# Performance work log

Measured on AMD Instinct MI355X. Metric: run time of the kernel, lower is better.

Reference implementation:

```python
import jax, jax.numpy as jnp
import numpy as np

H = 8  # n_heads (init_kwarg, closed over)


def setup_inputs() -> dict:
    key = jax.random.key(0)
    ks = jax.random.split(key, 5)
    B, T, D, L = 8, 4096, 512, 128
    # lecun_normal: std = 1/sqrt(fan_in), fan_in = first dim here
    X = jax.random.normal(ks[0], (B, T, D), dtype=jnp.float32)
    Wk = jax.random.normal(ks[1], (D, L), dtype=jnp.float32) / np.sqrt(D)
    Wq = jax.random.normal(ks[2], (D, L), dtype=jnp.float32) / np.sqrt(D)
    Wv = jax.random.normal(ks[3], (D, D), dtype=jnp.float32) / np.sqrt(D)
    o_proj = jax.random.normal(ks[4], (D, D), dtype=jnp.float32) / np.sqrt(D)
    return {"X": X, "Wk": Wk, "Wq": Wq, "Wv": Wv, "o_proj": o_proj}


def reference(X, Wk, Wq, Wv, o_proj):
    B, T, D = X.shape
    L = Wk.shape[1]
    Dh, Lh = D // H, L // H
    # time-major projections: (T, B, H, *)
    V = jnp.einsum('DM,BTD->TBM', Wv, X).reshape(T, B, H, Dh)
    Q = jnp.einsum('DL,BTD->TBL', Wq, X).reshape(T, B, H, Lh)
    K = jnp.einsum('DL,BTD->TBL', Wk, X).reshape(T, B, H, Lh)
    scale = jax.lax.rsqrt(jnp.array(Dh, dtype=jnp.float32))
    K_exp = jnp.exp(K * scale)                      # (T,B,H,Lh)
    alpha = jnp.cumsum(K_exp, axis=0)               # causal normalizer
    Qs = jax.nn.softmax(Q * scale, axis=-1) / alpha # (T,B,H,Lh)

    def step(carry, args):
        qs_t, ke_t, v_t = args
        carry = carry + jnp.einsum('bhl,bhd->bhld', ke_t, v_t)
        y_t = jnp.einsum('bhl,bhld->bhd', qs_t, carry)
        return carry, y_t

    init = jnp.zeros((B, H, Lh, Dh), dtype=X.dtype)
    _, y = jax.lax.scan(step, init, (Qs, K_exp, V), unroll=16)  # y: (T,B,H,Dh)
    # faithful to source: transpose(3,0,1,2) then reshape(B,T,D)
    y = y.transpose(3, 0, 1, 2).reshape(B, T, D)
    return y @ o_proj
```

## Files before the change

### kernel.cpp

```cpp
#include <hip/hip_runtime.h>
#include <hip/hip_bf16.h>

#define B_ 8
#define T_ 4096
#define D_ 512
#define L_ 128
#define H_ 8
#define Dh_ 64
#define Lh_ 16
#define M_ (B_*T_)
#define SCALE 0.125f

typedef __bf16 v8bf __attribute__((ext_vector_type(8)));
typedef float  v4f  __attribute__((ext_vector_type(4)));
typedef unsigned short u16;
typedef u16 v8u __attribute__((ext_vector_type(8)));

__device__ __forceinline__ float b2f(u16 h){
    unsigned int u = ((unsigned int)h) << 16;
    return __builtin_bit_cast(float, u);
}
__device__ __forceinline__ u16 f2bf(float f){
    unsigned int u = __builtin_bit_cast(unsigned int, f);
    u += 0x7FFFu + ((u >> 16) & 1u);
    return (u16)(u >> 16);
}

__global__ __launch_bounds__(256) void f32_to_bf16(
        const float* __restrict__ src, u16* __restrict__ dst)
{
    const size_t i = (size_t)blockIdx.x * 256 + threadIdx.x;
    const float4* s = (const float4*)src + i * 2;
    float4 a = s[0], b = s[1];
    v8u o;
    o[0] = f2bf(a.x); o[1] = f2bf(a.y); o[2] = f2bf(a.z); o[3] = f2bf(a.w);
    o[4] = f2bf(b.x); o[5] = f2bf(b.y); o[6] = f2bf(b.z); o[7] = f2bf(b.w);
    *((v8u*)dst + i) = o;
}

__global__ __launch_bounds__(256) void transpose_w(
        const float* __restrict__ src, u16* __restrict__ dst, int rows, int cols)
{
    __shared__ u16 tile[32][33];
    int tx = threadIdx.x, ty = threadIdx.y;
    int c0 = blockIdx.x * 32, r0 = blockIdx.y * 32;
    #pragma unroll
    for (int i = 0; i < 32; i += 8)
        tile[ty + i][tx] = f2bf(src[(size_t)(r0 + ty + i) * cols + c0 + tx]);
    __syncthreads();
    #pragma unroll
    for (int i = 0; i < 32; i += 8)
        dst[(size_t)(c0 + ty + i) * rows + r0 + tx] = tile[tx][ty + i];
}

template<int MODE>
__global__ __launch_bounds__(256) void gemm_mfma(
        const u16* __restrict__ A, const u16* __restrict__ Bt,
        float* __restrict__ Qo, u16* __restrict__ KEo,
        u16* __restrict__ Vo, float* __restrict__ OutF)
{
    __shared__ __align__(16) u16 As[128][48];
    __shared__ __align__(16) u16 Bs[128][48];
    const int tid  = threadIdx.x;
    const int wave = tid >> 6, lane = tid & 63;
    const int wm = wave >> 1, wn = wave & 1;
    const int lm = lane & 15, quad = lane >> 4;
    const int gm0 = blockIdx.x * 128, gn0 = blockIdx.y * 128;

    v4f acc[4][4];
    #pragma unroll
    for (int i = 0; i < 4; i++)
        #pragma unroll
        for (int j = 0; j < 4; j++)
            acc[i][j] = (v4f){0.f, 0.f, 0.f, 0.f};

    for (int kt = 0; kt < 16; ++kt) {
        const int k0 = kt * 32;
        #pragma unroll
        for (int rep = 0; rep < 2; ++rep) {
            int lin = tid + rep * 256;
            int r = lin >> 2, c8 = (lin & 3) * 8;
            *(v8u*)&As[r][c8] = *(const v8u*)&A [(size_t)(gm0 + r) * 512 + k0 + c8];
            *(v8u*)&Bs[r][c8] = *(const v8u*)&Bt[(size_t)(gn0 + r) * 512 + k0 + c8];
        }
        __syncthreads();
        v8bf af[4], bfr[4];
        #pragma unroll
        for (int mi = 0; mi < 4; mi++)
            af[mi] = *(const v8bf*)&As[wm * 64 + mi * 16 + lm][quad * 8];
        #pragma unroll
        for (int ni = 0; ni < 4; ni++)
            bfr[ni] = *(const v8bf*)&Bs[wn * 64 + ni * 16 + lm][quad * 8];
        #pragma unroll
        for (int mi = 0; mi < 4; mi++)
            #pragma unroll
            for (int ni = 0; ni < 4; ni++)
                acc[mi][ni] = __builtin_amdgcn_mfma_f32_16x16x32_bf16(
                                  af[mi], bfr[ni], acc[mi][ni], 0, 0, 0);
        __syncthreads();
    }

    #pragma unroll
    for (int mi = 0; mi < 4; mi++)
      #pragma unroll
      for (int ni = 0; ni < 4; ni++)
        #pragma unroll
        for (int i = 0; i < 4; i++) {
            int row = gm0 + wm * 64 + mi * 16 + quad * 4 + i;
            int col = gn0 + wn * 64 + ni * 16 + lm;
            float v = acc[mi][ni][i];
            if (MODE == 0) {
                if (col < 128)        Qo [(size_t)row * 128 + col]       = v;
                else if (col < 256)   KEo[(size_t)row * 128 + col - 128] = f2bf(__expf(v * SCALE));
                else                  Vo [(size_t)row * 512 + col - 256] = f2bf(v);
            } else {
                OutF[(size_t)row * 512 + col] = v;
            }
        }
}

__global__ __launch_bounds__(256, 2) void chunk_sums_mfma(
        const u16* __restrict__ KE, const u16* __restrict__ V,
        float* __restrict__ Mc, float* __restrict__ AB)
{
    struct CLDS { u16 KA[16][72]; u16 VT[64][72]; };
    __shared__ __align__(16) CLDS lds[4];
    const int tid = threadIdx.x, wave = tid >> 6, lane = tid & 63;
    const int lm = lane & 15, quad = lane >> 4;
    const int ch = blockIdx.x * 4 + wave;
    const int bh = ch >> 6, c = ch & 63, b = bh >> 3, h = bh & 7;
    const int t0 = b * T_ + c * 64;
    CLDS& L = lds[wave];

    {
        const u16* kp = KE + (size_t)(t0 + lane) * L_ + h * Lh_;
        v8u k0 = *(const v8u*)kp, k1 = *(const v8u*)(kp + 8);
        #pragma unroll
        for (int l = 0; l < 8; l++) L.KA[l][lane]     = k0[l];
        #pragma unroll
        for (int l = 0; l < 8; l++) L.KA[l + 8][lane] = k1[l];
        const u16* vp = V + (size_t)(t0 + lane) * D_ + h * Dh_;
        #pragma unroll
        for (int seg = 0; seg < 8; ++seg) {
            v8u pv = *(const v8u*)(vp + seg * 8);
            #pragma unroll
            for (int j = 0; j < 8; j++) L.VT[seg * 8 + j][lane] = pv[j];
        }
    }
    __syncthreads();

    v8bf ka[2];
    #pragma unroll
    for (int ki = 0; ki < 2; ki++)
        ka[ki] = *(const v8bf*)&L.KA[lm][ki * 32 + quad * 8];

    v8u onesu;
    #pragma unroll
    for (int j = 0; j < 8; j++) onesu[j] = 0x3F80;
    v8bf ones = __builtin_bit_cast(v8bf, onesu);

    v4f accL = (v4f){0.f, 0.f, 0.f, 0.f};
    accL = __builtin_amdgcn_mfma_f32_16x16x32_bf16(ka[0], ones, accL, 0, 0, 0);
    accL = __builtin_amdgcn_mfma_f32_16x16x32_bf16(ka[1], ones, accL, 0, 0, 0);

    v4f accM[4];
    #pragma unroll
    for (int nd = 0; nd < 4; nd++) accM[nd] = (v4f){0.f, 0.f, 0.f, 0.f};
    #pragma unroll
    for (int nd = 0; nd < 4; nd++)
        #pragma unroll
        for (int ki = 0; ki < 2; ki++) {
            v8bf vb = *(const v8bf*)&L.VT[nd * 16 + lm][ki * 32 + quad * 8];
            accM[nd] = __builtin_amdgcn_mfma_f32_16x16x32_bf16(ka[ki], vb, accM[nd], 0, 0, 0);
        }

    float* mcb = Mc + (size_t)ch * 1024;
    #pragma unroll
    for (int nd = 0; nd < 4; nd++)
        #pragma unroll
        for (int i = 0; i < 4; i++)
            mcb[(quad * 4 + i) * 64 + nd * 16 + lm] = accM[nd][i];
    if (lm == 0) {
        #pragma unroll
        for (int i = 0; i < 4; i++) AB[ch * 16 + quad * 4 + i] = accL[i];
    }
}

__global__ __launch_bounds__(256) void chunk_prefix(
        float* __restrict__ Mc, float* __restrict__ AB)
{
    const int bh = blockIdx.x >> 2, qq = blockIdx.x & 3;
    const int i = qq * 256 + threadIdx.x;
    float run = 0.f;
    for (int c = 0; c < 64; ++c) {
        size_t off = ((size_t)(bh * 64 + c)) * 1024 + i;
        float m = Mc[off]; Mc[off] = run; run += m;
    }
    if (qq == 0 && threadIdx.x < 16) {
        float r2 = 0.f; const int l = threadIdx.x;
        for (int c = 0; c < 64; ++c) {
            int off = (bh * 64 + c) * 16 + l;
            float a = AB[off]; AB[off] = r2; r2 += a;
        }
    }
}

__global__ __launch_bounds__(256, 2) void intra_mfma(
        const float* __restrict__ Q, const u16* __restrict__ KE,
        const u16* __restrict__ V, const float* __restrict__ Mc,
        const float* __restrict__ AB, u16* __restrict__ Y)
{
    struct ILDS {
        union {
            struct { u16 KA[16][72]; u16 Sc[16][72]; u16 qs[64][40]; } s;
            u16 p[64][72];
        } r;
        u16 VT[64][72];
    };
    __shared__ __align__(16) ILDS lds[4];
    const int tid = threadIdx.x, wave = tid >> 6, lane = tid & 63;
    const int lm = lane & 15, quad = lane >> 4;
    const int ch = blockIdx.x * 4 + wave;
    const int bh = ch >> 6, c = ch & 63, b = bh >> 3, h = bh & 7;
    const int t0 = b * T_ + c * 64;
    ILDS& L = lds[wave];

    {
        const u16* kp = KE + (size_t)(t0 + lane) * L_ + h * Lh_;
        v8u k0 = *(const v8u*)kp, k1 = *(const v8u*)(kp + 8);
        #pragma unroll
        for (int l = 0; l < 8; l++) L.r.s.KA[l][lane]     = k0[l];
        #pragma unroll
        for (int l = 0; l < 8; l++) L.r.s.KA[l + 8][lane] = k1[l];
        const u16* vp = V + (size_t)(t0 + lane) * D_ + h * Dh_;
        #pragma unroll
        for (int seg = 0; seg < 8; ++seg) {
            v8u pv = *(const v8u*)(vp + seg * 8);
            #pragma unroll
            for (int j = 0; j < 8; j++) L.VT[seg * 8 + j][lane] = pv[j];
        }
        const float* mcb = Mc + (size_t)ch * 1024;
        #pragma unroll
        for (int l = 0; l < 16; l++)
            L.r.s.Sc[l][lane] = f2bf(mcb[l * 64 + lane]);
        v8u z8;
        #pragma unroll
        for (int j = 0; j < 8; j++) z8[j] = 0;
        *(v8u*)&L.r.s.qs[lane][16] = z8;
        *(v8u*)&L.r.s.qs[lane][24] = z8;
    }
    const float ab = AB[ch * 16 + lm];
    __syncthreads();

    v4f acc_a[4];
    #pragma unroll
    for (int mi = 0; mi < 4; mi++) acc_a[mi] = (v4f){ab, ab, ab, ab};
    #pragma unroll
    for (int mi = 0; mi < 4; mi++)
        #pragma unroll
        for (int ki = 0; ki < 2; ki++) {
            if (ki == 1 && mi < 2) continue;
            v8u ta;
            #pragma unroll
            for (int j = 0; j < 8; j++)
                ta[j] = (ki * 32 + quad * 8 + j <= mi * 16 + lm) ? (u16)0x3F80 : (u16)0;
            v8bf kb = *(const v8bf*)&L.r.s.KA[lm][ki * 32 + quad * 8];
            acc_a[mi] = __builtin_amdgcn_mfma_f32_16x16x32_bf16(
                            __builtin_bit_cast(v8bf, ta), kb, acc_a[mi], 0, 0, 0);
        }

    #pragma unroll
    for (int mi = 0; mi < 4; mi++)
        #pragma unroll
        for (int i = 0; i < 4; i++) {
            int t = mi * 16 + quad * 4 + i;
            float qv = Q[(size_t)(t0 + t) * L_ + h * Lh_ + lm] * SCALE;
            float m = qv;
            #pragma unroll
            for (int off = 1; off < 16; off <<= 1) m = fmaxf(m, __shfl_xor(m, off));
            float e = __expf(qv - m);
            float s = e;
            #pragma unroll
            for (int off = 1; off < 16; off <<= 1) s += __shfl_xor(s, off);
            L.r.s.qs[t][lm] = f2bf(e / (s * acc_a[mi][i]));
        }
    __syncthreads();

    v8bf aq[4];
    #pragma unroll
    for (int mi = 0; mi < 4; mi++)
        aq[mi] = *(const v8bf*)&L.r.s.qs[mi * 16 + lm][quad * 8];

    v4f accP[4][4], accY[4][4];
    #pragma unroll
    for (int mi = 0; mi < 4; mi++)
        #pragma unroll
        for (int ni = 0; ni < 4; ni++) {
            accP[mi][ni] = (v4f){0.f, 0.f, 0.f, 0.f};
            accY[mi][ni] = (v4f){0.f, 0.f, 0.f, 0.f};
        }

    #pragma unroll
    for (int ni = 0; ni < 4; ni++) {
        v8u kbu;
        #pragma unroll
        for (int j = 0; j < 8; j++) kbu[j] = 0;
        if (quad < 2) {
            #pragma unroll
            for (int j = 0; j < 8; j++)
                kbu[j] = L.r.s.KA[quad * 8 + j][ni * 16 + lm];
        }
        v8bf kbf = __builtin_bit_cast(v8bf, kbu);
        #pragma unroll
        for (int mi = ni; mi < 4; mi++)
            accP[mi][ni] = __builtin_amdgcn_mfma_f32_16x16x32_bf16(
                               aq[mi], kbf, accP[mi][ni], 0, 0, 0);
    }
    #pragma unroll
    for (int nd = 0; nd < 4; nd++) {
        v8u scu;
        #pragma unroll
        for (int j = 0; j < 8; j++) scu[j] = 0;
        if (quad < 2) {
            #pragma unroll
            for (int j = 0; j < 8; j++)
                scu[j] = L.r.s.Sc[quad * 8 + j][nd * 16 + lm];
        }
        v8bf scf = __builtin_bit_cast(v8bf, scu);
        #pragma unroll
        for (int mi = 0; mi < 4; mi++)
            accY[mi][nd] = __builtin_amdgcn_mfma_f32_16x16x32_bf16(
                               aq[mi], scf, accY[mi][nd], 0, 0, 0);
    }
    __syncthreads();

    #pragma unroll
    for (int mi = 0; mi < 4; mi++)
        #pragma unroll
        for (int ni = 0; ni < 4; ni++)
            #pragma unroll
            for (int i = 0; i < 4; i++) {
                int t = mi * 16 + quad * 4 + i, tp = ni * 16 + lm;
                float pv = (ni < mi) ? accP[mi][ni][i]
                          : (ni == mi ? ((tp <= t) ? accP[mi][ni][i] : 0.f) : 0.f);
                L.r.p[t][tp] = f2bf(pv);
            }
    __syncthreads();

    v8bf vb[4][2];
    #pragma unroll
    for (int nd = 0; nd < 4; nd++)
        #pragma unroll
        for (int ki = 0; ki < 2; ki++)
            vb[nd][ki] = *(const v8bf*)&L.VT[nd * 16 + lm][ki * 32 + quad * 8];
    #pragma unroll
    for (int mi = 0; mi < 4; mi++)
        #pragma unroll
        for (int ki = 0; ki < 2; ki++) {
            if (ki == 1 && mi < 2) continue;
            v8bf pa = *(const v8bf*)&L.r.p[mi * 16 + lm][ki * 32 + quad * 8];
            #pragma unroll
            for (int nd = 0; nd < 4; nd++)
                accY[mi][nd] = __builtin_amdgcn_mfma_f32_16x16x32_bf16(
                                   pa, vb[nd][ki], accY[mi][nd], 0, 0, 0);
        }

    #pragma unroll
    for (int mi = 0; mi < 4; mi++)
        #pragma unroll
        for (int nd = 0; nd < 4; nd++)
            #pragma unroll
            for (int i = 0; i < 4; i++) {
                int t = mi * 16 + quad * 4 + i;
                Y[(((size_t)(c * 64 + t)) * 64 + bh) * 64 + nd * 16 + lm] =
                    f2bf(accY[mi][nd][i]);
            }
}

__global__ __launch_bounds__(64) void transpose_Y(
        const u16* __restrict__ Y, u16* __restrict__ Z)
{
    __shared__ __align__(16) u16 tile[64][72];
    const int g = blockIdx.x;
    const int t = threadIdx.x;
    const u16* yp = Y + ((size_t)(g * 64 + t)) * 64;
    #pragma unroll
    for (int seg = 0; seg < 8; ++seg)
        *(v8u*)&tile[t][seg * 8] = *(const v8u*)(yp + seg * 8);
    __syncthreads();
    const int d = t;
    u16* zp = Z + (size_t)d * 262144 + (size_t)g * 64;
    #pragma unroll
    for (int seg = 0; seg < 8; ++seg) {
        v8u pk;
        #pragma unroll
        for (int j = 0; j < 8; j++) pk[j] = tile[seg * 8 + j][d];
        *(v8u*)(zp + seg * 8) = pk;
    }
}

extern "C" void kernel_launch(void* const* d_in, const int* in_sizes, int n_in,
                              void* d_out, int out_size, void* d_ws, size_t ws_size,
                              hipStream_t stream)
{
    (void)in_sizes; (void)n_in; (void)out_size; (void)ws_size;
    const float* X  = (const float*)d_in[0];
    const float* Wk = (const float*)d_in[1];
    const float* Wq = (const float*)d_in[2];
    const float* Wv = (const float*)d_in[3];
    const float* Wo = (const float*)d_in[4];
    float* Out = (float*)d_out;

    char* p = (char*)d_ws;
    auto alloc = [&](size_t bytes) { char* r = p; p += (bytes + 255) & ~(size_t)255; return r; };
    u16*   Xb = (u16*)  alloc((size_t)M_ * 512 * 2);
    u16*   WT = (u16*)  alloc((size_t)768 * 512 * 2);
    u16*   OT = (u16*)  alloc((size_t)512 * 512 * 2);
    u16*   V  = (u16*)  alloc((size_t)M_ * 512 * 2);
    float* Mc = (float*)alloc((size_t)4096 * 1024 * 4);
    float* AB = (float*)alloc((size_t)4096 * 16 * 4);
    float* Q  = (float*)alloc((size_t)M_ * 128 * 4);
    u16*   KE = (u16*)  alloc((size_t)M_ * 128 * 2);
    u16*   Y  = (u16*)  alloc((size_t)M_ * 512 * 2);
    u16*   Z  = (u16*)Mc;

    f32_to_bf16<<<8192, 256, 0, stream>>>(X, Xb);

    dim3 tb(32, 8);
    transpose_w<<<dim3(4, 16),  tb, 0, stream>>>(Wq, WT + 0   * 512, 512, 128);
    transpose_w<<<dim3(4, 16),  tb, 0, stream>>>(Wk, WT + 128 * 512, 512, 128);
    transpose_w<<<dim3(16, 16), tb, 0, stream>>>(Wv, WT + 256 * 512, 512, 512);
    transpose_w<<<dim3(16, 16), tb, 0, stream>>>(Wo, OT,             512, 512);

    gemm_mfma<0><<<dim3(256, 6), 256, 0, stream>>>(Xb, WT, Q, KE, V, nullptr);
    chunk_sums_mfma<<<1024, 256, 0, stream>>>(KE, V, Mc, AB);
    chunk_prefix   <<<256,  256, 0, stream>>>(Mc, AB);
    intra_mfma     <<<1024, 256, 0, stream>>>(Q, KE, V, Mc, AB, Y);
    transpose_Y    <<<4096, 64,  0, stream>>>(Y, Z);
    gemm_mfma<1><<<dim3(256, 4), 256, 0, stream>>>(Z, OT, nullptr, nullptr, nullptr, Out);
}
```

Measured before the change: 285.5 us.

## Merge prep kernels, use direct global-to-LDS loads with swizzle, coalesce Y transpose

Five small preprocessing launches become one prep kernel that handles the X conversion and the four weight transposes by block index. The GEMM now loads tiles straight from global memory into LDS with global_load_lds, uses an XOR-swizzled 64-wide K tile, and halves the number of K iterations and barriers. transpose_Y is remapped so each thread writes contiguous 16-byte segments along the time axis, giving coalesced stores. This cuts launch overhead, register staging and LDS bank conflicts, but relies on the lane-to-LDS layout of global_load_lds matching the swizzle exactly.

```diff
diff --git a/kernel.cpp b/kernel.cpp
--- a/kernel.cpp
+++ b/kernel.cpp
@@ -26,31 +26,45 @@
     return (u16)(u >> 16);
 }
 
-__global__ __launch_bounds__(256) void f32_to_bf16(
-        const float* __restrict__ src, u16* __restrict__ dst)
-{
-    const size_t i = (size_t)blockIdx.x * 256 + threadIdx.x;
-    const float4* s = (const float4*)src + i * 2;
-    float4 a = s[0], b = s[1];
-    v8u o;
-    o[0] = f2bf(a.x); o[1] = f2bf(a.y); o[2] = f2bf(a.z); o[3] = f2bf(a.w);
-    o[4] = f2bf(b.x); o[5] = f2bf(b.y); o[6] = f2bf(b.z); o[7] = f2bf(b.w);
-    *((v8u*)dst + i) = o;
-}
-
-__global__ __launch_bounds__(256) void transpose_w(
-        const float* __restrict__ src, u16* __restrict__ dst, int rows, int cols)
-{
+__device__ __forceinline__ void gload16(const u16* g, u16* l) {
+    __builtin_amdgcn_global_load_lds(
+        (const __attribute__((address_space(1))) unsigned int*)(g),
+        (__attribute__((address_space(3))) unsigned int*)(l), 16, 0, 0);
+}
+
+__global__ __launch_bounds__(256) void prep(
+        const float* __restrict__ X,  const float* __restrict__ Wq,
+        const float* __restrict__ Wk, const float* __restrict__ Wv,
+        const float* __restrict__ Wo,
+        u16* __restrict__ Xb, u16* __restrict__ WT, u16* __restrict__ OT)
+{
+    int bid = blockIdx.x;
+    if (bid < 8192) {
+        const size_t i = (size_t)bid * 256 + threadIdx.x;
+        const float4* s = (const float4*)X + i * 2;
+        float4 a = s[0], b = s[1];
+        v8u o;
+        o[0] = f2bf(a.x); o[1] = f2bf(a.y); o[2] = f2bf(a.z); o[3] = f2bf(a.w);
+        o[4] = f2bf(b.x); o[5] = f2bf(b.y); o[6] = f2bf(b.z); o[7] = f2bf(b.w);
+        *((v8u*)Xb + i) = o;
+        return;
+    }
+    bid -= 8192;
+    const float* src; u16* dst; int cols, bx, by;
+    if (bid < 64)       { src = Wq; dst = WT;             cols = 128; bx = bid & 3;  by = bid >> 2; }
+    else if (bid < 128) { src = Wk; dst = WT + 128 * 512; cols = 128; bid -= 64;  bx = bid & 3;  by = bid >> 2; }
+    else if (bid < 384) { src = Wv; dst = WT + 256 * 512; cols = 512; bid -= 128; bx = bid & 15; by = bid >> 4; }
+    else                { src = Wo; dst = OT;             cols = 512; bid -= 384; bx = bid & 15; by = bid >> 4; }
     __shared__ u16 tile[32][33];
-    int tx = threadIdx.x, ty = threadIdx.y;
-    int c0 = blockIdx.x * 32, r0 = blockIdx.y * 32;
+    const int tx = threadIdx.x & 31, ty = threadIdx.x >> 5;
+    const int c0 = bx * 32, r0 = by * 32;
     #pragma unroll
     for (int i = 0; i < 32; i += 8)
         tile[ty + i][tx] = f2bf(src[(size_t)(r0 + ty + i) * cols + c0 + tx]);
     __syncthreads();
     #pragma unroll
     for (int i = 0; i < 32; i += 8)
-        dst[(size_t)(c0 + ty + i) * rows + r0 + tx] = tile[tx][ty + i];
+        dst[(size_t)(c0 + ty + i) * 512 + r0 + tx] = tile[tx][ty + i];
 }
 
 template<int MODE>
@@ -59,14 +73,17 @@
         float* __restrict__ Qo, u16* __restrict__ KEo,
         u16* __restrict__ Vo, float* __restrict__ OutF)
 {
-    __shared__ __align__(16) u16 As[128][48];
-    __shared__ __align__(16) u16 Bs[128][48];
+    __shared__ __align__(16) u16 As[128 * 64];
+    __shared__ __align__(16) u16 Bs[128 * 64];
     const int tid  = threadIdx.x;
     const int wave = tid >> 6, lane = tid & 63;
     const int wm = wave >> 1, wn = wave & 1;
     const int lm = lane & 15, quad = lane >> 4;
     const int gm0 = blockIdx.x * 128, gn0 = blockIdx.y * 128;
 
+    const int srow0 = wave * 32 + (lane >> 3);
+    const int sg    = lane & 7;
+
     v4f acc[4][4];
     #pragma unroll
     for (int i = 0; i < 4; i++)
@@ -74,29 +91,35 @@
         for (int j = 0; j < 4; j++)
             acc[i][j] = (v4f){0.f, 0.f, 0.f, 0.f};
 
-    for (int kt = 0; kt < 16; ++kt) {
-        const int k0 = kt * 32;
-        #pragma unroll
-        for (int rep = 0; rep < 2; ++rep) {
-            int lin = tid + rep * 256;
-            int r = lin >> 2, c8 = (lin & 3) * 8;
-            *(v8u*)&As[r][c8] = *(const v8u*)&A [(size_t)(gm0 + r) * 512 + k0 + c8];
-            *(v8u*)&Bs[r][c8] = *(const v8u*)&Bt[(size_t)(gn0 + r) * 512 + k0 + c8];
+    for (int kt = 0; kt < 8; ++kt) {
+        const int k0 = kt * 64;
+        #pragma unroll
+        for (int r = 0; r < 4; ++r) {
+            const int row = srow0 + r * 8;
+            const int col = ((sg ^ (row & 7)) << 3) + k0;
+            gload16(&A [(size_t)(gm0 + row) * 512 + col], &As[(wave * 4 + r) * 512]);
+            gload16(&Bt[(size_t)(gn0 + row) * 512 + col], &Bs[(wave * 4 + r) * 512]);
         }
         __syncthreads();
-        v8bf af[4], bfr[4];
-        #pragma unroll
-        for (int mi = 0; mi < 4; mi++)
-            af[mi] = *(const v8bf*)&As[wm * 64 + mi * 16 + lm][quad * 8];
-        #pragma unroll
-        for (int ni = 0; ni < 4; ni++)
-            bfr[ni] = *(const v8bf*)&Bs[wn * 64 + ni * 16 + lm][quad * 8];
-        #pragma unroll
-        for (int mi = 0; mi < 4; mi++)
-            #pragma unroll
-            for (int ni = 0; ni < 4; ni++)
-                acc[mi][ni] = __builtin_amdgcn_mfma_f32_16x16x32_bf16(
-                                  af[mi], bfr[ni], acc[mi][ni], 0, 0, 0);
+        v8bf af[2][4], bfr[2][4];
+        #pragma unroll
+        for (int ks = 0; ks < 2; ks++)
+            #pragma unroll
+            for (int mi = 0; mi < 4; mi++) {
+                const int g  = ks * 4 + quad;
+                const int ra = wm * 64 + mi * 16 + lm;
+                const int rb = wn * 64 + mi * 16 + lm;
+                af [ks][mi] = *(const v8bf*)&As[ra * 64 + ((g ^ (ra & 7)) << 3)];
+                bfr[ks][mi] = *(const v8bf*)&Bs[rb * 64 + ((g ^ (rb & 7)) << 3)];
+            }
+        #pragma unroll
+        for (int ks = 0; ks < 2; ks++)
+            #pragma unroll
+            for (int mi = 0; mi < 4; mi++)
+                #pragma unroll
+                for (int ni = 0; ni < 4; ni++)
+                    acc[mi][ni] = __builtin_amdgcn_mfma_f32_16x16x32_bf16(
+                                      af[ks][mi], bfr[ks][ni], acc[mi][ni], 0, 0, 0);
         __syncthreads();
     }
 
@@ -381,21 +404,20 @@
         const u16* __restrict__ Y, u16* __restrict__ Z)
 {
     __shared__ __align__(16) u16 tile[64][72];
-    const int g = blockIdx.x;
-    const int t = threadIdx.x;
-    const u16* yp = Y + ((size_t)(g * 64 + t)) * 64;
+    const int g = blockIdx.x, t = threadIdx.x;
+    const u16* yp = Y + (size_t)(g * 64 + t) * 64;
     #pragma unroll
     for (int seg = 0; seg < 8; ++seg)
         *(v8u*)&tile[t][seg * 8] = *(const v8u*)(yp + seg * 8);
     __syncthreads();
-    const int d = t;
-    u16* zp = Z + (size_t)d * 262144 + (size_t)g * 64;
-    #pragma unroll
-    for (int seg = 0; seg < 8; ++seg) {
+    const int cl = t & 7, dq = t >> 3;
+    #pragma unroll
+    for (int p = 0; p < 8; ++p) {
+        const int dh = p * 8 + dq;
         v8u pk;
         #pragma unroll
-        for (int j = 0; j < 8; j++) pk[j] = tile[seg * 8 + j][d];
-        *(v8u*)(zp + seg * 8) = pk;
+        for (int j = 0; j < 8; j++) pk[j] = tile[cl * 8 + j][dh];
+        *(v8u*)&Z[(size_t)dh * 262144 + (size_t)g * 64 + cl * 8] = pk;
     }
 }
 
@@ -424,13 +446,7 @@
     u16*   Y  = (u16*)  alloc((size_t)M_ * 512 * 2);
     u16*   Z  = (u16*)Mc;
 
-    f32_to_bf16<<<8192, 256, 0, stream>>>(X, Xb);
-
-    dim3 tb(32, 8);
-    transpose_w<<<dim3(4, 16),  tb, 0, stream>>>(Wq, WT + 0   * 512, 512, 128);
-    transpose_w<<<dim3(4, 16),  tb, 0, stream>>>(Wk, WT + 128 * 512, 512, 128);
-    transpose_w<<<dim3(16, 16), tb, 0, stream>>>(Wv, WT + 256 * 512, 512, 512);
-    transpose_w<<<dim3(16, 16), tb, 0, stream>>>(Wo, OT,             512, 512);
+    prep<<<8832, 256, 0, stream>>>(X, Wq, Wk, Wv, Wo, Xb, WT, OT);
 
     gemm_mfma<0><<<dim3(256, 6), 256, 0, stream>>>(Xb, WT, Q, KE, V, nullptr);
     chunk_sums_mfma<<<1024, 256, 0, stream>>>(KE, V, Mc, AB);
```

New measurement: 248.7 us. 12.9% less time.
